# Kernel optimization log

Hardware: AMD Instinct MI355X
Metric: run time of the kernel (lower is better)

## Reference

```python
import jax, jax.numpy as jnp
import numpy as np

N_NODES = 100000
N_EDGES = 3200000


def setup_inputs() -> dict:
    key = jax.random.key(0)
    ks = jax.random.split(key, 10)
    inp = {
        "x": jax.random.normal(ks[0], (N_NODES, 16), dtype=jnp.float32),
        "edge_index": jax.random.randint(ks[1], (2, N_EDGES), 0, N_NODES, dtype=jnp.int64),
        "W1": jax.random.normal(ks[2], (16, 32), dtype=jnp.float32) * 0.25,
        "b1": jax.random.normal(ks[3], (32,), dtype=jnp.float32) * 0.02,
        "W2": jax.random.normal(ks[4], (32, 32), dtype=jnp.float32) * 0.18,
        "b2": jax.random.normal(ks[5], (32,), dtype=jnp.float32) * 0.02,
        "Wl1": jax.random.normal(ks[6], (32, 32), dtype=jnp.float32) * 0.18,
        "bl1": jax.random.normal(ks[7], (32,), dtype=jnp.float32) * 0.02,
        "Wl4": jax.random.normal(ks[8], (32, 1), dtype=jnp.float32) * 0.18,
        "bl4": jax.random.normal(ks[9], (1,), dtype=jnp.float32) * 0.02,
    }
    return inp


def _gcn_norm(edge_index, n_nodes):
    # PyG GCNConv default: add self-loops, symmetric normalization D^-1/2 A_hat D^-1/2.
    loops = jnp.arange(n_nodes, dtype=edge_index.dtype)
    row = jnp.concatenate([edge_index[0], loops])  # source j
    col = jnp.concatenate([edge_index[1], loops])  # target i
    deg = jax.ops.segment_sum(jnp.ones_like(col, dtype=jnp.float32), col, num_segments=n_nodes)
    dinv = jnp.where(deg > 0, jax.lax.rsqrt(deg), 0.0)
    norm = dinv[row] * dinv[col]  # [E + N]
    return row, col, norm


def _gcn_conv(x, W, b, row, col, norm, n_nodes):
    h = x @ W                                   # [N, out] small GEMM
    msgs = h[row] * norm[:, None]               # irregular gather, [E+N, out]
    out = jax.ops.segment_sum(msgs, col, num_segments=n_nodes)  # scatter-add
    return out + b


def reference(x, edge_index, W1, b1, W2, b2, Wl1, bl1, Wl4, bl4):
    n = x.shape[0]
    row, col, norm = _gcn_norm(edge_index, n)
    h = jax.nn.relu(_gcn_conv(x, W1, b1, row, col, norm, n))
    h = jax.nn.relu(_gcn_conv(h, W2, b2, row, col, norm, n))
    h = jax.nn.relu(h @ Wl1 + bl1)
    return h @ Wl4 + bl4  # [N, 1]
```

## Files before the change

### kernel.cpp

```cpp
#include <hip/hip_runtime.h>
#include <hip/hip_fp16.h>
#include <math.h>


#define BN 256
#define BSH 8
#define NBUF 512
#define EPB 4096
#define EPT 8
#define CMAX 10240
#define SLDS 1536

__global__ void __launch_bounds__(512)
bucket_scatter(const int* __restrict__ row, const int* __restrict__ col,
               int* __restrict__ gCursor, int* __restrict__ packed,
               int E, int NB, int C) {
    __shared__ int hist[NBUF];
    __shared__ int base[NBUF];
    int t = threadIdx.x;
    int blockBase = blockIdx.x * EPB;
    for (int i = t; i < NB; i += 512) hist[i] = 0;
    __syncthreads();
    int pay[EPT];
    int meta[EPT];
#pragma unroll
    for (int k = 0; k < EPT; ++k) {
        int e = blockBase + k * 512 + t;
        if (e < E) {
            int c = col[e];
            int b = c >> BSH;
            int r = atomicAdd(&hist[b], 1);
            pay[k] = (row[e] << BSH) | (c & (BN - 1));
            meta[k] = (b << 16) | r;
        } else {
            meta[k] = -1;
        }
    }
    __syncthreads();
    for (int b = t; b < NB; b += 512) {
        int c = hist[b];
        base[b] = c ? atomicAdd(&gCursor[b], c) : 0;
    }
    __syncthreads();
#pragma unroll
    for (int k = 0; k < EPT; ++k) {
        int m = meta[k];
        if (m >= 0) {
            int b = m >> 16;
            int off = base[b] + (m & 0xFFFF);
            if (off < C)
                packed[(size_t)b * C + off] = pay[k];
        }
    }
}

__global__ void __launch_bounds__(1024)
bucket_finalize(const int* __restrict__ packed, const int* __restrict__ gCursor,
                int2* __restrict__ rowRange, int* __restrict__ rowMid,
                float* __restrict__ dinv, int* __restrict__ srcs,
                const float4* __restrict__ x4, __half* __restrict__ xs,
                int N, int C, int halfN) {
    __shared__ int cnt[BN * 2];
    __shared__ int cur[BN * 2];
    __shared__ float sdv[BN];
    __shared__ int wsum[16];
    __shared__ int sorted[CMAX];
    int bkt = blockIdx.x;
    int t = threadIdx.x;
    int nodeBase = bkt << BSH;
    if (t < BN * 2) cnt[t] = 0;
    __syncthreads();
    int beg = bkt * C;
    int end = beg + min(gCursor[bkt], C);
    int m = end - beg;
    for (int e = beg + t; e < end; e += 1024) {
        int w = packed[e];
        int key = ((w & (BN - 1)) << 1) | ((w >> BSH) >= halfN ? 1 : 0);
        atomicAdd(&cnt[key], 1);
    }
    __syncthreads();
    int c0 = (t < BN) ? cnt[2 * t] : 0;
    int c1 = (t < BN) ? cnt[2 * t + 1] : 0;
    int s = c0 + c1;
    int lane = t & 63, wv = t >> 6;
    int v = s;
#pragma unroll
    for (int off = 1; off < 64; off <<= 1) {
        int u = __shfl_up(v, off);
        if (lane >= off) v += u;
    }
    if (lane == 63) wsum[wv] = v;
    __syncthreads();
    int addv = 0;
#pragma unroll
    for (int w = 0; w < 16; ++w) addv += (w < wv) ? wsum[w] : 0;
    v += addv;
    if (t < BN) {
        int p = v - s;
        cur[2 * t] = p;
        cur[2 * t + 1] = p + c0;
        float d = rsqrtf((float)s + 1.0f);
        sdv[t] = d;
        int n = nodeBase + t;
        if (n < N) {
            rowRange[n] = make_int2(beg + p, beg + p + s);
            rowMid[n] = beg + p + c0;
            dinv[n] = d;
        }
    }
    __syncthreads();
    bool useLds = (m <= CMAX);
    for (int e = beg + t; e < end; e += 1024) {
        int w = packed[e];
        int src = w >> BSH;
        int key = ((w & (BN - 1)) << 1) | (src >= halfN ? 1 : 0);
        int pos = atomicAdd(&cur[key], 1);
        if (useLds) sorted[pos] = src;
        else        srcs[beg + pos] = src;
    }
    __syncthreads();
    if (useLds)
        for (int i = t; i < m; i += 1024) srcs[beg + i] = sorted[i];
    {
        int n = t >> 1, hf = t & 1;
        int g = nodeBase + n;
        if (t < BN * 2 && g < N) {
            float d = sdv[n];
            float4 va = x4[(size_t)g * 4 + hf * 2];
            float4 vb = x4[(size_t)g * 4 + hf * 2 + 1];
            __half2 h0 = __floats2half2_rn(va.x * d, va.y * d);
            __half2 h1 = __floats2half2_rn(va.z * d, va.w * d);
            __half2 h2 = __floats2half2_rn(vb.x * d, vb.y * d);
            __half2 h3 = __floats2half2_rn(vb.z * d, vb.w * d);
            uint4 u;
            u.x = *(unsigned*)&h0; u.y = *(unsigned*)&h1;
            u.z = *(unsigned*)&h2; u.w = *(unsigned*)&h3;
            *(uint4*)(xs + (size_t)g * 16 + hf * 8) = u;
        }
    }
}

__device__ __forceinline__ void acc8(float* a, uint4 u) {
    float2 f;
    f = __half22float2(*(const __half2*)&u.x); a[0] += f.x; a[1] += f.y;
    f = __half22float2(*(const __half2*)&u.y); a[2] += f.x; a[3] += f.y;
    f = __half22float2(*(const __half2*)&u.z); a[4] += f.x; a[5] += f.y;
    f = __half22float2(*(const __half2*)&u.w); a[6] += f.x; a[7] += f.y;
}

__device__ __forceinline__ void gather_pipe(float* a, const int* __restrict__ idx,
                                            const __half* __restrict__ tbl,
                                            int rowHalves, int off8,
                                            int first, int limit, int stride) {
    if (first >= limit) return;
    int cntE = (limit - first + stride - 1) / stride;
    int last = limit - 1;
    int i0 = idx[first];
    int i1 = idx[min(first + stride, last)];
    int i2 = idx[min(first + stride * 2, last)];
    int i3 = idx[min(first + stride * 3, last)];
    uint4 f0 = *(const uint4*)(tbl + (size_t)i0 * rowHalves + off8 * 8);
    uint4 f1 = *(const uint4*)(tbl + (size_t)i1 * rowHalves + off8 * 8);
    uint4 f2 = *(const uint4*)(tbl + (size_t)i2 * rowHalves + off8 * 8);
    uint4 f3 = *(const uint4*)(tbl + (size_t)i3 * rowHalves + off8 * 8);
    int i = 0;
    for (; i + 4 <= cntE; i += 4) {
        int n0 = idx[min(first + stride * (i + 4), last)];
        int n1 = idx[min(first + stride * (i + 5), last)];
        int n2 = idx[min(first + stride * (i + 6), last)];
        int n3 = idx[min(first + stride * (i + 7), last)];
        acc8(a, f0); f0 = *(const uint4*)(tbl + (size_t)n0 * rowHalves + off8 * 8);
        acc8(a, f1); f1 = *(const uint4*)(tbl + (size_t)n1 * rowHalves + off8 * 8);
        acc8(a, f2); f2 = *(const uint4*)(tbl + (size_t)n2 * rowHalves + off8 * 8);
        acc8(a, f3); f3 = *(const uint4*)(tbl + (size_t)n3 * rowHalves + off8 * 8);
    }
    int r = cntE - i;
    if (r > 0) acc8(a, f0);
    if (r > 1) acc8(a, f1);
    if (r > 2) acc8(a, f2);
}

__global__ void __launch_bounds__(256)
gather_conv1(const int2* __restrict__ rowRange, const int* __restrict__ srcs,
             const __half* __restrict__ xs, const float* __restrict__ dinv,
             const float* __restrict__ W1, const float* __restrict__ b1,
             __half* __restrict__ hs1, int N) {
    __shared__ float A[32][17];
    __shared__ float sW[512];
    __shared__ float sb[32];
    __shared__ int sIdx[SLDS];
    int t = threadIdx.x;
    for (int i = t; i < 512; i += 256) sW[i] = W1[i];
    if (t < 32) sb[t] = b1[t];
    int node0 = blockIdx.x * 32;
    int lastN = min(node0 + 31, N - 1);
    int base = rowRange[node0].x;
    int tot = rowRange[lastN].y - base;
    bool useLds = (tot <= SLDS);
    if (useLds)
        for (int i = t; i < tot; i += 256) sIdx[i] = srcs[base + i];
    __syncthreads();
    int tt = blockIdx.x * 256 + t;
    int node = tt >> 3, q = tt & 7, ln = t >> 3;
    int eo = q >> 1, hf = q & 1;
    float a[8] = {0.f, 0.f, 0.f, 0.f, 0.f, 0.f, 0.f, 0.f};
    float di = 0.f;
    if (node < N) {
        int2 rr = rowRange[node];
        if (useLds)
            gather_pipe(a, sIdx, xs, 16, hf, rr.x - base + eo, rr.y - base, 4);
        else
            gather_pipe(a, srcs, xs, 16, hf, rr.x + eo, rr.y, 4);
        if (eo == 0)
            acc8(a, *(const uint4*)(xs + (size_t)node * 16 + hf * 8));
        di = dinv[node];
    }
#pragma unroll
    for (int j = 0; j < 8; ++j) {
        a[j] += __shfl_xor(a[j], 2);
        a[j] += __shfl_xor(a[j], 4);
        a[j] *= di;
    }
    if (eo == 0) {
#pragma unroll
        for (int j = 0; j < 8; ++j) A[ln][hf * 8 + j] = a[j];
    }
    __syncthreads();
    if (node < N) {
        int k0 = q * 4;
        float acc[4];
#pragma unroll
        for (int j = 0; j < 4; ++j) acc[j] = sb[k0 + j];
#pragma unroll
        for (int c = 0; c < 16; ++c) {
            float ac = A[ln][c];
#pragma unroll
            for (int j = 0; j < 4; ++j) acc[j] += ac * sW[c * 32 + k0 + j];
        }
        __half2 h0 = __floats2half2_rn(di * fmaxf(acc[0], 0.f),
                                       di * fmaxf(acc[1], 0.f));
        __half2 h1 = __floats2half2_rn(di * fmaxf(acc[2], 0.f),
                                       di * fmaxf(acc[3], 0.f));
        uint2 u;
        u.x = *(unsigned*)&h0; u.y = *(unsigned*)&h1;
        *(uint2*)(hs1 + (size_t)node * 32 + k0) = u;
    }
}

__global__ void __launch_bounds__(256)
gather_conv2_head(const int2* __restrict__ rowRange, const int* __restrict__ rowMid,
                  const int* __restrict__ srcs, const __half* __restrict__ hs1,
                  const float* __restrict__ dinv,
                  const float* __restrict__ W2, const float* __restrict__ b2,
                  const float* __restrict__ Wl1, const float* __restrict__ bl1,
                  const float* __restrict__ Wl4, const float* __restrict__ bl4,
                  float* __restrict__ out, int N) {
    __shared__ float A[32][33];
    __shared__ float sW2[1024];
    __shared__ float sWl1[1024];
    __shared__ float sb2[32], sbl1[32], sWl4[32];
    __shared__ float sbl4;
    __shared__ int sIdx[SLDS];
    int t = threadIdx.x;
    for (int i = t; i < 1024; i += 256) { sW2[i] = W2[i]; sWl1[i] = Wl1[i]; }
    if (t < 32) { sb2[t] = b2[t]; sbl1[t] = bl1[t]; sWl4[t] = Wl4[t]; }
    if (t == 0) sbl4 = bl4[0];
    int node0 = blockIdx.x * 32;
    int lastN = min(node0 + 31, N - 1);
    int base = rowRange[node0].x;
    int tot = rowRange[lastN].y - base;
    bool useLds = (tot <= SLDS);
    if (useLds)
        for (int i = t; i < tot; i += 256) sIdx[i] = srcs[base + i];
    __syncthreads();
    int tt = blockIdx.x * 256 + t;
    int node = tt >> 3, q = tt & 7, ln = t >> 3;
    int eo = q >> 2, part = q & 3;
    float a[8] = {0.f, 0.f, 0.f, 0.f, 0.f, 0.f, 0.f, 0.f};
    if (node < N) {
        int2 rr = rowRange[node];
        int mid = rowMid[node];
        if (useLds) {
            gather_pipe(a, sIdx, hs1, 32, part, rr.x - base + eo, mid - base, 2);
            gather_pipe(a, sIdx, hs1, 32, part, mid - base + eo, rr.y - base, 2);
        } else {
            gather_pipe(a, srcs, hs1, 32, part, rr.x + eo, mid, 2);
            gather_pipe(a, srcs, hs1, 32, part, mid + eo, rr.y, 2);
        }
        if (eo == 0)
            acc8(a, *(const uint4*)(hs1 + (size_t)node * 32 + part * 8));
    }
#pragma unroll
    for (int j = 0; j < 8; ++j) a[j] += __shfl_xor(a[j], 4);
    if (node < N && eo == 0) {
        float di = dinv[node];
#pragma unroll
        for (int j = 0; j < 8; ++j) a[j] *= di;
#pragma unroll
        for (int j = 0; j < 8; ++j) A[ln][part * 8 + j] = a[j];
    }
    __syncthreads();
    int k0 = q * 4;
    float h2[4];
#pragma unroll
    for (int j = 0; j < 4; ++j) h2[j] = sb2[k0 + j];
#pragma unroll
    for (int c = 0; c < 32; ++c) {
        float ac = A[ln][c];
#pragma unroll
        for (int j = 0; j < 4; ++j) h2[j] += ac * sW2[c * 32 + k0 + j];
    }
#pragma unroll
    for (int j = 0; j < 4; ++j) h2[j] = fmaxf(h2[j], 0.f);
    __syncthreads();
#pragma unroll
    for (int j = 0; j < 4; ++j) A[ln][k0 + j] = h2[j];
    __syncthreads();
    float h3[4];
#pragma unroll
    for (int j = 0; j < 4; ++j) h3[j] = sbl1[k0 + j];
#pragma unroll
    for (int c = 0; c < 32; ++c) {
        float ac = A[ln][c];
#pragma unroll
        for (int j = 0; j < 4; ++j) h3[j] += ac * sWl1[c * 32 + k0 + j];
    }
    float p = 0.f;
#pragma unroll
    for (int j = 0; j < 4; ++j) p += fmaxf(h3[j], 0.f) * sWl4[k0 + j];
    p += __shfl_xor(p, 1);
    p += __shfl_xor(p, 2);
    p += __shfl_xor(p, 4);
    if (q == 0 && node < N) out[node] = p + sbl4;
}

extern "C" void kernel_launch(void* const* d_in, const int* in_sizes, int n_in,
                              void* d_out, int out_size, void* d_ws, size_t ws_size,
                              hipStream_t stream) {
    const float* x   = (const float*)d_in[0];
    const int*   ei  = (const int*)d_in[1];
    const float* W1  = (const float*)d_in[2];
    const float* b1  = (const float*)d_in[3];
    const float* W2  = (const float*)d_in[4];
    const float* b2  = (const float*)d_in[5];
    const float* Wl1 = (const float*)d_in[6];
    const float* bl1 = (const float*)d_in[7];
    const float* Wl4 = (const float*)d_in[8];
    const float* bl4 = (const float*)d_in[9];
    float* out = (float*)d_out;

    const int N = in_sizes[0] / 16;
    const int E = in_sizes[1] / 2;
    const int* row = ei;
    const int* col = ei + E;
    const int NB = (N + BN - 1) >> BSH;
    const int halfN = N / 2;
    int C = (E + NB - 1) / NB;
    C = (C * 9 + 7) / 8;
    C = (C + 63) & ~63;

    char* ws = (char*)d_ws;
    auto align = [](size_t v) { return (v + 511) & ~(size_t)511; };
    size_t o = 0;
    int*    gCursor  = (int*)(ws + o);    o = align(o + (size_t)NBUF * 4);
    int2*   rowRange = (int2*)(ws + o);   o = align(o + (size_t)N * 8);
    int*    rowMid   = (int*)(ws + o);    o = align(o + (size_t)N * 4);
    float*  dinv     = (float*)(ws + o);  o = align(o + (size_t)N * 4);
    int*    packed   = (int*)(ws + o);    o = align(o + (size_t)NB * C * 4);
    int*    srcs     = (int*)(ws + o);    o = align(o + (size_t)NB * C * 4);
    __half* xs       = (__half*)(ws + o); o = align(o + (size_t)N * 16 * 2);
    __half* hs1      = (__half*)(ws + o); o = align(o + (size_t)N * 32 * 2);

    const int BLK = 256;
    int gridSc = (E + EPB - 1) / EPB;
    int gridG8 = (N * 8 + BLK - 1) / BLK;

    hipMemsetAsync(gCursor, 0, (size_t)NBUF * 4, stream);
    bucket_scatter<<<gridSc, 512, 0, stream>>>(row, col, gCursor, packed, E, NB, C);
    bucket_finalize<<<NB, 1024, 0, stream>>>(packed, gCursor, rowRange, rowMid, dinv,
                                             srcs, (const float4*)x, xs, N, C, halfN);

    gather_conv1<<<gridG8, BLK, 0, stream>>>(rowRange, srcs, xs, dinv, W1, b1, hs1, N);

    gather_conv2_head<<<gridG8, BLK, 0, stream>>>(rowRange, rowMid, srcs, hs1, dinv,
                                                  W2, b2, Wl1, bl1,
                                                  Wl4, bl4, out, N);
}
```

Baseline: 187.9 us.

## Sort nodes by degree within each bucket to balance gather work per wavefront

Within each 256-node bucket, nodes are counting-sorted by descending in-degree and their CSR segments are laid out in that order. A perm array maps each slot back to the original node, so the gather kernels handle nodes of similar degree together and write outputs through the permutation. The aim is to reduce load imbalance and divergence among the 8-thread groups and wavefronts in the gather loops. It adds extra scans and atomics to finalize, an extra perm read per node, and scattered output writes. The LDS index staging limit is also raised.

```diff
diff --git a/kernel.cpp b/kernel.cpp
--- a/kernel.cpp
+++ b/kernel.cpp
@@ -9,7 +9,7 @@
 #define EPB 4096
 #define EPT 8
 #define CMAX 10240
-#define SLDS 1536
+#define SLDS 2048
 
 __global__ void __launch_bounds__(512)
 bucket_scatter(const int* __restrict__ row, const int* __restrict__ col,
@@ -57,18 +57,25 @@
 __global__ void __launch_bounds__(1024)
 bucket_finalize(const int* __restrict__ packed, const int* __restrict__ gCursor,
                 int2* __restrict__ rowRange, int* __restrict__ rowMid,
-                float* __restrict__ dinv, int* __restrict__ srcs,
+                float* __restrict__ dinv, int* __restrict__ perm,
+                int* __restrict__ srcs,
                 const float4* __restrict__ x4, __half* __restrict__ xs,
                 int N, int C, int halfN) {
     __shared__ int cnt[BN * 2];
     __shared__ int cur[BN * 2];
     __shared__ float sdv[BN];
-    __shared__ int wsum[16];
+    __shared__ int cntD[256];
+    __shared__ int curD[256];
+    __shared__ int sByRank[256];
+    __shared__ int prefByRank[256];
+    __shared__ int wsumD[4];
+    __shared__ int wsumR[4];
     __shared__ int sorted[CMAX];
     int bkt = blockIdx.x;
     int t = threadIdx.x;
     int nodeBase = bkt << BSH;
     if (t < BN * 2) cnt[t] = 0;
+    if (t < 256) { cntD[t] = 0; sByRank[t] = 0; }
     __syncthreads();
     int beg = bkt * C;
     int end = beg + min(gCursor[bkt], C);
@@ -83,30 +90,63 @@
     int c1 = (t < BN) ? cnt[2 * t + 1] : 0;
     int s = c0 + c1;
     int lane = t & 63, wv = t >> 6;
-    int v = s;
-#pragma unroll
-    for (int off = 1; off < 64; off <<= 1) {
-        int u = __shfl_up(v, off);
-        if (lane >= off) v += u;
-    }
-    if (lane == 63) wsum[wv] = v;
-    __syncthreads();
-    int addv = 0;
-#pragma unroll
-    for (int w = 0; w < 16; ++w) addv += (w < wv) ? wsum[w] : 0;
-    v += addv;
-    if (t < BN) {
-        int p = v - s;
+    bool real = (t < BN) && (nodeBase + t < N);
+    int bin = 255 - min(s, 255);
+    if (real) atomicAdd(&cntD[bin], 1);
+    __syncthreads();
+    {
+        int bc = (t < 256) ? cntD[t] : 0;
+        int vv = bc;
+#pragma unroll
+        for (int off = 1; off < 64; off <<= 1) {
+            int u = __shfl_up(vv, off);
+            if (lane >= off) vv += u;
+        }
+        if (t < 256 && lane == 63) wsumD[wv] = vv;
+        __syncthreads();
+        if (t < 256) {
+            int add = 0;
+#pragma unroll
+            for (int w = 0; w < 4; ++w) add += (w < wv) ? wsumD[w] : 0;
+            curD[t] = vv + add - bc;
+        }
+    }
+    __syncthreads();
+    int r = 0;
+    if (real) {
+        r = atomicAdd(&curD[bin], 1);
+        sByRank[r] = s;
+    }
+    __syncthreads();
+    {
+        int val = (t < 256) ? sByRank[t] : 0;
+        int vv = val;
+#pragma unroll
+        for (int off = 1; off < 64; off <<= 1) {
+            int u = __shfl_up(vv, off);
+            if (lane >= off) vv += u;
+        }
+        if (t < 256 && lane == 63) wsumR[wv] = vv;
+        __syncthreads();
+        if (t < 256) {
+            int add = 0;
+#pragma unroll
+            for (int w = 0; w < 4; ++w) add += (w < wv) ? wsumR[w] : 0;
+            prefByRank[t] = vv + add - val;
+        }
+    }
+    __syncthreads();
+    if (real) {
+        int p = prefByRank[r];
         cur[2 * t] = p;
         cur[2 * t + 1] = p + c0;
         float d = rsqrtf((float)s + 1.0f);
         sdv[t] = d;
-        int n = nodeBase + t;
-        if (n < N) {
-            rowRange[n] = make_int2(beg + p, beg + p + s);
-            rowMid[n] = beg + p + c0;
-            dinv[n] = d;
-        }
+        int slot = nodeBase + r;
+        rowRange[slot] = make_int2(beg + p, beg + p + s);
+        rowMid[slot] = beg + p + c0;
+        dinv[slot] = d;
+        perm[slot] = nodeBase + t;
     }
     __syncthreads();
     bool useLds = (m <= CMAX);
@@ -181,7 +221,8 @@
 }
 
 __global__ void __launch_bounds__(256)
-gather_conv1(const int2* __restrict__ rowRange, const int* __restrict__ srcs,
+gather_conv1(const int2* __restrict__ rowRange, const int* __restrict__ perm,
+             const int* __restrict__ srcs,
              const __half* __restrict__ xs, const float* __restrict__ dinv,
              const float* __restrict__ W1, const float* __restrict__ b1,
              __half* __restrict__ hs1, int N) {
@@ -192,28 +233,30 @@
     int t = threadIdx.x;
     for (int i = t; i < 512; i += 256) sW[i] = W1[i];
     if (t < 32) sb[t] = b1[t];
-    int node0 = blockIdx.x * 32;
-    int lastN = min(node0 + 31, N - 1);
-    int base = rowRange[node0].x;
-    int tot = rowRange[lastN].y - base;
+    int slot0 = blockIdx.x * 32;
+    int lastS = min(slot0 + 31, N - 1);
+    int base = rowRange[slot0].x;
+    int tot = rowRange[lastS].y - base;
     bool useLds = (tot <= SLDS);
     if (useLds)
         for (int i = t; i < tot; i += 256) sIdx[i] = srcs[base + i];
     __syncthreads();
     int tt = blockIdx.x * 256 + t;
-    int node = tt >> 3, q = tt & 7, ln = t >> 3;
+    int slot = tt >> 3, q = tt & 7, ln = t >> 3;
     int eo = q >> 1, hf = q & 1;
     float a[8] = {0.f, 0.f, 0.f, 0.f, 0.f, 0.f, 0.f, 0.f};
     float di = 0.f;
-    if (node < N) {
-        int2 rr = rowRange[node];
+    int orig = 0;
+    if (slot < N) {
+        orig = perm[slot];
+        int2 rr = rowRange[slot];
         if (useLds)
             gather_pipe(a, sIdx, xs, 16, hf, rr.x - base + eo, rr.y - base, 4);
         else
             gather_pipe(a, srcs, xs, 16, hf, rr.x + eo, rr.y, 4);
         if (eo == 0)
-            acc8(a, *(const uint4*)(xs + (size_t)node * 16 + hf * 8));
-        di = dinv[node];
+            acc8(a, *(const uint4*)(xs + (size_t)orig * 16 + hf * 8));
+        di = dinv[slot];
     }
 #pragma unroll
     for (int j = 0; j < 8; ++j) {
@@ -226,7 +269,7 @@
         for (int j = 0; j < 8; ++j) A[ln][hf * 8 + j] = a[j];
     }
     __syncthreads();
-    if (node < N) {
+    if (slot < N) {
         int k0 = q * 4;
         float acc[4];
 #pragma unroll
@@ -243,12 +286,13 @@
                                        di * fmaxf(acc[3], 0.f));
         uint2 u;
         u.x = *(unsigned*)&h0; u.y = *(unsigned*)&h1;
-        *(uint2*)(hs1 + (size_t)node * 32 + k0) = u;
+        *(uint2*)(hs1 + (size_t)orig * 32 + k0) = u;
     }
 }
 
 __global__ void __launch_bounds__(256)
 gather_conv2_head(const int2* __restrict__ rowRange, const int* __restrict__ rowMid,
+                  const int* __restrict__ perm,
                   const int* __restrict__ srcs, const __half* __restrict__ hs1,
                   const float* __restrict__ dinv,
                   const float* __restrict__ W2, const float* __restrict__ b2,
@@ -265,21 +309,23 @@
     for (int i = t; i < 1024; i += 256) { sW2[i] = W2[i]; sWl1[i] = Wl1[i]; }
     if (t < 32) { sb2[t] = b2[t]; sbl1[t] = bl1[t]; sWl4[t] = Wl4[t]; }
     if (t == 0) sbl4 = bl4[0];
-    int node0 = blockIdx.x * 32;
-    int lastN = min(node0 + 31, N - 1);
-    int base = rowRange[node0].x;
-    int tot = rowRange[lastN].y - base;
+    int slot0 = blockIdx.x * 32;
+    int lastS = min(slot0 + 31, N - 1);
+    int base = rowRange[slot0].x;
+    int tot = rowRange[lastS].y - base;
     bool useLds = (tot <= SLDS);
     if (useLds)
         for (int i = t; i < tot; i += 256) sIdx[i] = srcs[base + i];
     __syncthreads();
     int tt = blockIdx.x * 256 + t;
-    int node = tt >> 3, q = tt & 7, ln = t >> 3;
+    int slot = tt >> 3, q = tt & 7, ln = t >> 3;
     int eo = q >> 2, part = q & 3;
     float a[8] = {0.f, 0.f, 0.f, 0.f, 0.f, 0.f, 0.f, 0.f};
-    if (node < N) {
-        int2 rr = rowRange[node];
-        int mid = rowMid[node];
+    int orig = 0;
+    if (slot < N) {
+        orig = perm[slot];
+        int2 rr = rowRange[slot];
+        int mid = rowMid[slot];
         if (useLds) {
             gather_pipe(a, sIdx, hs1, 32, part, rr.x - base + eo, mid - base, 2);
             gather_pipe(a, sIdx, hs1, 32, part, mid - base + eo, rr.y - base, 2);
@@ -288,12 +334,12 @@
             gather_pipe(a, srcs, hs1, 32, part, mid + eo, rr.y, 2);
         }
         if (eo == 0)
-            acc8(a, *(const uint4*)(hs1 + (size_t)node * 32 + part * 8));
+            acc8(a, *(const uint4*)(hs1 + (size_t)orig * 32 + part * 8));
     }
 #pragma unroll
     for (int j = 0; j < 8; ++j) a[j] += __shfl_xor(a[j], 4);
-    if (node < N && eo == 0) {
-        float di = dinv[node];
+    if (slot < N && eo == 0) {
+        float di = dinv[slot];
 #pragma unroll
         for (int j = 0; j < 8; ++j) a[j] *= di;
 #pragma unroll
@@ -331,7 +377,7 @@
     p += __shfl_xor(p, 1);
     p += __shfl_xor(p, 2);
     p += __shfl_xor(p, 4);
-    if (q == 0 && node < N) out[node] = p + sbl4;
+    if (q == 0 && slot < N) out[orig] = p + sbl4;
 }
 
 extern "C" void kernel_launch(void* const* d_in, const int* in_sizes, int n_in,
@@ -366,6 +412,7 @@
     int2*   rowRange = (int2*)(ws + o);   o = align(o + (size_t)N * 8);
     int*    rowMid   = (int*)(ws + o);    o = align(o + (size_t)N * 4);
     float*  dinv     = (float*)(ws + o);  o = align(o + (size_t)N * 4);
+    int*    perm     = (int*)(ws + o);    o = align(o + (size_t)(N + BN) * 4);
     int*    packed   = (int*)(ws + o);    o = align(o + (size_t)NB * C * 4);
     int*    srcs     = (int*)(ws + o);    o = align(o + (size_t)NB * C * 4);
     __half* xs       = (__half*)(ws + o); o = align(o + (size_t)N * 16 * 2);
@@ -378,11 +425,13 @@
     hipMemsetAsync(gCursor, 0, (size_t)NBUF * 4, stream);
     bucket_scatter<<<gridSc, 512, 0, stream>>>(row, col, gCursor, packed, E, NB, C);
     bucket_finalize<<<NB, 1024, 0, stream>>>(packed, gCursor, rowRange, rowMid, dinv,
-                                             srcs, (const float4*)x, xs, N, C, halfN);
-
-    gather_conv1<<<gridG8, BLK, 0, stream>>>(rowRange, srcs, xs, dinv, W1, b1, hs1, N);
-
-    gather_conv2_head<<<gridG8, BLK, 0, stream>>>(rowRange, rowMid, srcs, hs1, dinv,
-                                                  W2, b2, Wl1, bl1,
+                                             perm, srcs, (const float4*)x, xs,
+                                             N, C, halfN);
+
+    gather_conv1<<<gridG8, BLK, 0, stream>>>(rowRange, perm, srcs, xs, dinv,
+                                             W1, b1, hs1, N);
+
+    gather_conv2_head<<<gridG8, BLK, 0, stream>>>(rowRange, rowMid, perm, srcs, hs1,
+                                                  dinv, W2, b2, Wl1, bl1,
                                                   Wl4, bl4, out, N);
 }
```

Result: slower. 200.0 us (+6.5%).
